# Performance work log

Hardware: AMD Instinct MI355X
Metric: run time of the kernel (lower is better)

The kernel has to match this reference:

```python
import jax, jax.numpy as jnp
import numpy as np

N, INC, INN, OUTC, OUTN, MAXD = 16, 32, 65536, 32, 8192, 16

def setup_inputs() -> dict:
    key = jax.random.key(0)
    ks = jax.random.split(key, 7)
    x = jax.random.normal(ks[0], (N, INC, INN), jnp.float32)
    A = jax.random.randint(ks[1], (OUTN, MAXD), 0, INN, dtype=jnp.int64)
    weight = 0.2 * jax.random.normal(ks[2], (INC, INN), jnp.float32)
    # normalize=True with fixed degree MAXD -> mask = 1/maxD everywhere
    mask = jnp.ones((OUTN, MAXD, 1), jnp.float32) / MAXD
    mask_weight = 0.2 * jax.random.normal(ks[3], (OUTN, MAXD, 1), jnp.float32)
    ct_weight = jax.random.normal(ks[4], (OUTC, INC), jnp.float32) / np.sqrt(INC)
    ct_bias = 0.02 * jax.random.normal(ks[5], (OUTC,), jnp.float32)
    bias = 0.2 * jax.random.normal(ks[6], (OUTC, OUTN), jnp.float32)
    return {"x": x, "A": A, "weight": weight, "mask": mask,
            "mask_weight": mask_weight, "ct_weight": ct_weight,
            "ct_bias": ct_bias, "bias": bias}

def reference(x, A, weight, mask, mask_weight, ct_weight, ct_bias, bias):
    n, inc, inn = x.shape
    outn, maxD = A.shape
    # per-input-node channel scaling, then lay out as (inn, N*inc) feature table
    feat = (x * weight).reshape(n * inc, inn).T            # (inn, N*inc)
    emb = feat[A]                                          # (outn, maxD, N*inc) gather
    w = mask_weight * mask                                 # (outn, maxD, 1)
    pooled = (w * emb).reshape(outn, maxD, n, inc).sum(axis=1)  # (outn, N, inc)
    almost_y = jnp.einsum('onc,dc->ond', pooled, ct_weight) + ct_bias  # (outn, N, outc)
    return almost_y.transpose(1, 2, 0) + bias              # (N, outc, outn)
```

## Files before the change

### kernel.cpp

```cpp
#include <hip/hip_runtime.h>
#include <hip/hip_bf16.h>

#define NN    16
#define INC   32
#define INN   65536
#define OUTC  32
#define OUTN  8192
#define MAXD  16
#define NC    512

__global__ __launch_bounds__(256) void transpose_scale_kernel(
    const float* __restrict__ x,
    const float* __restrict__ weight,
    __hip_bfloat16* __restrict__ feat)
{
    __shared__ float tile[64][65];
    const int l  = threadIdx.x;
    const int j0 = blockIdx.x * 64;
    const int r0 = blockIdx.y * 64;

    #pragma unroll
    for (int it = 0; it < 16; ++it) {
        int idx = it * 256 + l;
        int rl  = idx >> 6;
        int jl  = idx & 63;
        int r   = r0 + rl;
        int j   = j0 + jl;
        int c   = r & 31;
        tile[rl][jl] = x[(size_t)r * INN + j] * weight[(size_t)c * INN + j];
    }
    __syncthreads();

    #pragma unroll
    for (int it = 0; it < 8; ++it) {
        int jl = it * 8 + (l >> 5);
        int rp = l & 31;
        float v0 = tile[2 * rp][jl];
        float v1 = tile[2 * rp + 1][jl];
        __hip_bfloat162 p;
        p.x = __float2bfloat16(v0);
        p.y = __float2bfloat16(v1);
        *reinterpret_cast<__hip_bfloat162*>(
            feat + (size_t)(j0 + jl) * NC + (r0 + 2 * rp)) = p;
    }
}

#define OTILE 16

__global__ __launch_bounds__(256) void gather_gemm_kernel(
    const __hip_bfloat16* __restrict__ feat,
    const int*   __restrict__ A,
    const float* __restrict__ mask,
    const float* __restrict__ mw,
    const float* __restrict__ ctw,
    const float* __restrict__ ctb,
    const float* __restrict__ bias,
    float*       __restrict__ out)
{
    __shared__ float pooled[OTILE][NC];
    __shared__ float ctl[32 * 33];

    const int l  = threadIdx.x;
    const int o0 = blockIdx.x * OTILE;

    for (int i = l; i < 32 * 32; i += 256) {
        int dout = i >> 5, c = i & 31;
        ctl[dout * 33 + c] = ctw[i];
    }

    for (int o = 0; o < OTILE; ++o) {
        const int oo = o0 + o;
        float a0 = 0.f, a1 = 0.f;
        #pragma unroll
        for (int d = 0; d < MAXD; ++d) {
            int   j = A[oo * MAXD + d] & (INN - 1);
            float w = mw[oo * MAXD + d] * mask[oo * MAXD + d];
            __hip_bfloat162 p = *reinterpret_cast<const __hip_bfloat162*>(
                feat + (size_t)j * NC + 2 * l);
            a0 += w * __bfloat162float(p.x);
            a1 += w * __bfloat162float(p.y);
        }
        *reinterpret_cast<float2*>(&pooled[o][2 * l]) = make_float2(a0, a1);
    }
    __syncthreads();

    const int dout = l & 31;
    const float cb = ctb[dout];
    #pragma unroll
    for (int h = 0; h < 2; ++h) {
        const int n = (l >> 5) + 8 * h;
        float vals[OTILE];
        #pragma unroll
        for (int o = 0; o < OTILE; ++o) {
            float s = cb;
            #pragma unroll
            for (int c = 0; c < 32; ++c)
                s += pooled[o][n * 32 + c] * ctl[dout * 33 + c];
            vals[o] = s + bias[(size_t)dout * OUTN + o0 + o];
        }
        float4* outp = reinterpret_cast<float4*>(
            out + ((size_t)(n * 32 + dout)) * OUTN + o0);
        #pragma unroll
        for (int q = 0; q < 4; ++q)
            outp[q] = make_float4(vals[4*q], vals[4*q+1], vals[4*q+2], vals[4*q+3]);
    }
}

extern "C" void kernel_launch(void* const* d_in, const int* in_sizes, int n_in,
                              void* d_out, int out_size, void* d_ws, size_t ws_size,
                              hipStream_t stream)
{
    const float* x      = (const float*)d_in[0];
    const int*   A      = (const int*)  d_in[1];
    const float* weight = (const float*)d_in[2];
    const float* mask   = (const float*)d_in[3];
    const float* mw     = (const float*)d_in[4];
    const float* ctw    = (const float*)d_in[5];
    const float* ctb    = (const float*)d_in[6];
    const float* bias   = (const float*)d_in[7];
    float* out = (float*)d_out;

    __hip_bfloat16* feat = (__hip_bfloat16*)d_ws;

    dim3 gA(INN / 64, NC / 64);
    transpose_scale_kernel<<<gA, 256, 0, stream>>>(x, weight, feat);

    gather_gemm_kernel<<<OUTN / OTILE, 256, 0, stream>>>(
        feat, A, mask, mw, ctw, ctb, bias, out);
}
```

Before: 290.7 us.

## Vectorize transpose and gather memory accesses, keep ct weights in registers

```diff
diff --git a/kernel.cpp b/kernel.cpp
--- a/kernel.cpp
+++ b/kernel.cpp
@@ -9,10 +9,12 @@
 #define MAXD  16
 #define NC    512
 
+typedef __attribute__((ext_vector_type(8))) unsigned short ushort8;
+
 __global__ __launch_bounds__(256) void transpose_scale_kernel(
     const float* __restrict__ x,
     const float* __restrict__ weight,
-    __hip_bfloat16* __restrict__ feat)
+    unsigned short* __restrict__ feat)
 {
     __shared__ float tile[64][65];
     const int l  = threadIdx.x;
@@ -20,35 +22,41 @@
     const int r0 = blockIdx.y * 64;
 
     #pragma unroll
-    for (int it = 0; it < 16; ++it) {
+    for (int it = 0; it < 4; ++it) {
         int idx = it * 256 + l;
-        int rl  = idx >> 6;
-        int jl  = idx & 63;
+        int rl  = idx >> 4;
+        int jj  = idx & 15;
         int r   = r0 + rl;
-        int j   = j0 + jl;
         int c   = r & 31;
-        tile[rl][jl] = x[(size_t)r * INN + j] * weight[(size_t)c * INN + j];
+        int j   = j0 + jj * 4;
+        float4 xv = *reinterpret_cast<const float4*>(x + (size_t)r * INN + j);
+        float4 wv = *reinterpret_cast<const float4*>(weight + (size_t)c * INN + j);
+        tile[jj * 4 + 0][rl] = xv.x * wv.x;
+        tile[jj * 4 + 1][rl] = xv.y * wv.y;
+        tile[jj * 4 + 2][rl] = xv.z * wv.z;
+        tile[jj * 4 + 3][rl] = xv.w * wv.w;
     }
     __syncthreads();
 
     #pragma unroll
-    for (int it = 0; it < 8; ++it) {
-        int jl = it * 8 + (l >> 5);
-        int rp = l & 31;
-        float v0 = tile[2 * rp][jl];
-        float v1 = tile[2 * rp + 1][jl];
-        __hip_bfloat162 p;
-        p.x = __float2bfloat16(v0);
-        p.y = __float2bfloat16(v1);
-        *reinterpret_cast<__hip_bfloat162*>(
-            feat + (size_t)(j0 + jl) * NC + (r0 + 2 * rp)) = p;
+    for (int p = 0; p < 2; ++p) {
+        int jl = p * 32 + (l >> 3);
+        int rs = (l & 7) * 8;
+        ushort8 pk;
+        #pragma unroll
+        for (int k = 0; k < 8; ++k) {
+            float v = tile[jl][rs + k];
+            pk[k] = __bfloat16_as_ushort(__float2bfloat16(v));
+        }
+        *reinterpret_cast<ushort8*>(
+            feat + (size_t)(j0 + jl) * NC + r0 + rs) = pk;
     }
 }
 
 #define OTILE 16
 
 __global__ __launch_bounds__(256) void gather_gemm_kernel(
-    const __hip_bfloat16* __restrict__ feat,
+    const unsigned short* __restrict__ feat,
     const int*   __restrict__ A,
     const float* __restrict__ mask,
     const float* __restrict__ mw,
@@ -58,34 +66,41 @@
     float*       __restrict__ out)
 {
     __shared__ float pooled[OTILE][NC];
-    __shared__ float ctl[32 * 33];
+    const int l    = threadIdx.x;
+    const int wave = l >> 6;
+    const int lane = l & 63;
+    const int o0   = blockIdx.x * OTILE;
 
-    const int l  = threadIdx.x;
-    const int o0 = blockIdx.x * OTILE;
+    const int dout = l & 31;
+    float ctr[32];
+    #pragma unroll
+    for (int q = 0; q < 8; ++q)
+        *reinterpret_cast<float4*>(&ctr[4 * q]) =
+            *reinterpret_cast<const float4*>(ctw + dout * 32 + 4 * q);
+    const float cb = ctb[dout];
 
-    for (int i = l; i < 32 * 32; i += 256) {
-        int dout = i >> 5, c = i & 31;
-        ctl[dout * 33 + c] = ctw[i];
-    }
-
-    for (int o = 0; o < OTILE; ++o) {
+    #pragma unroll
+    for (int i = 0; i < 4; ++i) {
+        const int o  = wave * 4 + i;
         const int oo = o0 + o;
-        float a0 = 0.f, a1 = 0.f;
+        float acc[8] = {0.f, 0.f, 0.f, 0.f, 0.f, 0.f, 0.f, 0.f};
         #pragma unroll
         for (int d = 0; d < MAXD; ++d) {
             int   j = A[oo * MAXD + d] & (INN - 1);
             float w = mw[oo * MAXD + d] * mask[oo * MAXD + d];
-            __hip_bfloat162 p = *reinterpret_cast<const __hip_bfloat162*>(
-                feat + (size_t)j * NC + 2 * l);
-            a0 += w * __bfloat162float(p.x);
-            a1 += w * __bfloat162float(p.y);
+            ushort8 p = *reinterpret_cast<const ushort8*>(
+                feat + (size_t)j * NC + lane * 8);
+            #pragma unroll
+            for (int k = 0; k < 8; ++k)
+                acc[k] += w * __uint_as_float((unsigned)p[k] << 16);
         }
-        *reinterpret_cast<float2*>(&pooled[o][2 * l]) = make_float2(a0, a1);
+        *reinterpret_cast<float4*>(&pooled[o][lane * 8]) =
+            make_float4(acc[0], acc[1], acc[2], acc[3]);
+        *reinterpret_cast<float4*>(&pooled[o][lane * 8 + 4]) =
+            make_float4(acc[4], acc[5], acc[6], acc[7]);
     }
     __syncthreads();
 
-    const int dout = l & 31;
-    const float cb = ctb[dout];
     #pragma unroll
     for (int h = 0; h < 2; ++h) {
         const int n = (l >> 5) + 8 * h;
@@ -94,8 +109,12 @@
         for (int o = 0; o < OTILE; ++o) {
             float s = cb;
             #pragma unroll
-            for (int c = 0; c < 32; ++c)
-                s += pooled[o][n * 32 + c] * ctl[dout * 33 + c];
+            for (int q = 0; q < 8; ++q) {
+                float4 pv = *reinterpret_cast<const float4*>(
+                    &pooled[o][n * 32 + 4 * q]);
+                s += pv.x * ctr[4 * q + 0] + pv.y * ctr[4 * q + 1]
+                   + pv.z * ctr[4 * q + 2] + pv.w * ctr[4 * q + 3];
+            }
             vals[o] = s + bias[(size_t)dout * OUTN + o0 + o];
         }
         float4* outp = reinterpret_cast<float4*>(
@@ -120,7 +139,7 @@
     const float* bias   = (const float*)d_in[7];
     float* out = (float*)d_out;
 
-    __hip_bfloat16* feat = (__hip_bfloat16*)d_ws;
+    unsigned short* feat = (unsigned short*)d_ws;
 
     dim3 gA(INN / 64, NC / 64);
     transpose_scale_kernel<<<gA, 256, 0, stream>>>(x, weight, feat);
```

New measurement: 258.7 us. -11.0%, faster.
